# Kernel tuning notes

Measured on AMD Instinct MI355X. Metric: run time of the kernel, lower is better.

The kernel has to match this reference:

```python
import jax, jax.numpy as jnp
import numpy as np

B, S, H = 4, 4096, 2880
E, K = 32, 4


def setup_inputs() -> dict:
    key = jax.random.key(0)
    k1, k2 = jax.random.split(key)
    hidden_states = jax.random.normal(k1, (B, S, H), dtype=jnp.float32)
    # router weight, scaled like a typical init (std ~ 1/sqrt(H))
    weight = jax.random.normal(k2, (E, H), dtype=jnp.float32) / np.sqrt(H)
    bias = jnp.zeros((E,), dtype=jnp.float32)
    return {"hidden_states": hidden_states, "weight": weight, "bias": bias}


def reference(hidden_states, weight, bias):
    b, s, h = hidden_states.shape
    x = hidden_states.reshape(-1, h)                     # [T, H]
    logits = jnp.einsum('th,eh->te', x, weight) + bias   # [T, E]
    # select top-k logits (sorted descending), then softmax over the subset
    topk_logits, topk_idx = jax.lax.top_k(logits, K)     # [T, K]
    topk_weight = jax.nn.softmax(topk_logits.astype(jnp.float32), axis=-1)
    return topk_idx, topk_weight
```

## Files before the change

### kernel.cpp

```cpp
#include <hip/hip_runtime.h>
#include <math.h>

#define H_DIM 2880
#define E_NUM 32
#define TOPK 4
#define TT 256
#define HCHUNK 360
#define NCH 8
#define KS 20
#define NS (HCHUNK / KS)

#define GLD16(gp, lp)                                                  \
    __builtin_amdgcn_global_load_lds(                                  \
        (const __attribute__((address_space(1))) void*)(gp),           \
        (__attribute__((address_space(3))) void*)(lp), 16, 0, 0)

__global__ void transpose_w(const float* __restrict__ w, float* __restrict__ wt) {
    __shared__ float tile[32][33];
    const int h0 = blockIdx.x * 32;
    const int tx = threadIdx.x;
    const int ty = threadIdx.y;
    tile[tx][ty] = w[ty * H_DIM + h0 + tx];
    __syncthreads();
    wt[(h0 + ty) * E_NUM + tx] = tile[ty][tx];
}

__global__ __launch_bounds__(256, 2) void partial_logits(
    const float* __restrict__ x, const float* __restrict__ wt,
    float* __restrict__ part, int T) {
    __shared__ float xs[2][TT * KS];
    const int tid = threadIdx.x;
    const int t0 = blockIdx.x * TT;
    const int k0 = blockIdx.y * HCHUNK;
    const int wave = tid >> 6, lane = tid & 63;

    const float* g[5];
    int ldsoff[5];
#pragma unroll
    for (int i = 0; i < 5; ++i) {
        int f = wave * 320 + i * 64 + lane;
        int r = f / 5, c = f % 5;
        g[i] = x + (size_t)(t0 + r) * H_DIM + k0 + c * 4;
        ldsoff[i] = f * 4;
    }

    float acc[E_NUM];
#pragma unroll
    for (int e = 0; e < E_NUM; ++e) acc[e] = 0.0f;

    const float4* wt4 = (const float4*)wt;

#pragma unroll
    for (int i = 0; i < 5; ++i) GLD16(g[i], &xs[0][ldsoff[i]]);

    for (int s = 0; s < NS; ++s) {
        __syncthreads();
        if (s + 1 < NS) {
#pragma unroll
            for (int i = 0; i < 5; ++i)
                GLD16(g[i] + (size_t)(s + 1) * KS, &xs[(s + 1) & 1][ldsoff[i]]);
        }

        const float* xrow = &xs[s & 1][tid * KS];
        const int kbase = k0 + s * KS;
#pragma unroll
        for (int kk = 0; kk < KS / 4; ++kk) {
            float4 xv = *(const float4*)&xrow[kk * 4];
#pragma unroll
            for (int c = 0; c < 4; ++c) {
                float xk = (&xv.x)[c];
                int kg = kbase + kk * 4 + c;
#pragma unroll
                for (int j = 0; j < 8; ++j) {
                    float4 w4 = wt4[kg * 8 + j];
                    acc[j * 4 + 0] += xk * w4.x;
                    acc[j * 4 + 1] += xk * w4.y;
                    acc[j * 4 + 2] += xk * w4.z;
                    acc[j * 4 + 3] += xk * w4.w;
                }
            }
        }
    }

    float4* out4 = (float4*)(part + ((size_t)blockIdx.y * T + t0 + tid) * E_NUM);
#pragma unroll
    for (int j = 0; j < 8; ++j)
        out4[j] = make_float4(acc[j * 4 + 0], acc[j * 4 + 1], acc[j * 4 + 2], acc[j * 4 + 3]);
}

__global__ void topk_softmax(const float* __restrict__ part,
                             const float* __restrict__ bias,
                             float* __restrict__ out, int T) {
    const int t = blockIdx.x * 64 + threadIdx.x;
    if (t >= T) return;

    float logit[E_NUM];
    const float4* b4 = (const float4*)bias;
#pragma unroll
    for (int j = 0; j < 8; ++j) {
        float4 b = b4[j];
        logit[j * 4 + 0] = b.x; logit[j * 4 + 1] = b.y;
        logit[j * 4 + 2] = b.z; logit[j * 4 + 3] = b.w;
    }
    for (int hc = 0; hc < NCH; ++hc) {
        const float4* p4 = (const float4*)(part + ((size_t)hc * T + t) * E_NUM);
#pragma unroll
        for (int j = 0; j < 8; ++j) {
            float4 p = p4[j];
            logit[j * 4 + 0] += p.x; logit[j * 4 + 1] += p.y;
            logit[j * 4 + 2] += p.z; logit[j * 4 + 3] += p.w;
        }
    }

    int idx[TOPK];
    float val[TOPK];
#pragma unroll
    for (int k = 0; k < TOPK; ++k) {
        float best = -INFINITY;
        int bi = 0;
#pragma unroll
        for (int e = 0; e < E_NUM; ++e) {
            bool taken = false;
            for (int p = 0; p < k; ++p) taken = taken || (idx[p] == e);
            float v = logit[e];
            if (!taken && v > best) { best = v; bi = e; }
        }
        idx[k] = bi;
        val[k] = best;
    }

    float ex[TOPK], sum = 0.0f;
#pragma unroll
    for (int k = 0; k < TOPK; ++k) { ex[k] = expf(val[k] - val[0]); sum += ex[k]; }
    float inv = 1.0f / sum;

#pragma unroll
    for (int k = 0; k < TOPK; ++k) {
        out[(size_t)t * 4 + k] = (float)idx[k];
        out[(size_t)T * 4 + (size_t)t * 4 + k] = ex[k] * inv;
    }
}

extern "C" void kernel_launch(void* const* d_in, const int* in_sizes, int n_in,
                              void* d_out, int out_size, void* d_ws, size_t ws_size,
                              hipStream_t stream) {
    const float* x    = (const float*)d_in[0];
    const float* w    = (const float*)d_in[1];
    const float* bias = (const float*)d_in[2];
    float* out = (float*)d_out;

    const int T = in_sizes[0] / H_DIM;

    float* part = (float*)d_ws;
    float* wt = part + (size_t)NCH * T * E_NUM;

    transpose_w<<<dim3(H_DIM / 32), dim3(32, 32), 0, stream>>>(w, wt);
    partial_logits<<<dim3(T / TT, NCH), 256, 0, stream>>>(x, wt, part, T);
    topk_softmax<<<dim3((T + 63) / 64), 64, 0, stream>>>(part, bias, out, T);
}
```

Measured before the change: 318.8 us.

## Compute two tokens per thread with wide weight loads and parallelize partial reduction

```diff
diff --git a/kernel.cpp b/kernel.cpp
--- a/kernel.cpp
+++ b/kernel.cpp
@@ -4,11 +4,13 @@
 #define H_DIM 2880
 #define E_NUM 32
 #define TOPK 4
-#define TT 256
-#define HCHUNK 360
-#define NCH 8
-#define KS 20
-#define NS (HCHUNK / KS)
+#define NCH 16
+#define HCHUNK 180
+#define TB 512
+#define KS 12
+#define NS 15
+
+typedef float vf16 __attribute__((ext_vector_type(16)));
 
 #define GLD16(gp, lp)                                                  \
     __builtin_amdgcn_global_load_lds(                                  \
@@ -28,116 +30,138 @@
 __global__ __launch_bounds__(256, 2) void partial_logits(
     const float* __restrict__ x, const float* __restrict__ wt,
     float* __restrict__ part, int T) {
-    __shared__ float xs[2][TT * KS];
+    __shared__ float xs[2][TB * KS];
     const int tid = threadIdx.x;
-    const int t0 = blockIdx.x * TT;
+    const int t0 = blockIdx.x * TB;
     const int k0 = blockIdx.y * HCHUNK;
     const int wave = tid >> 6, lane = tid & 63;
 
-    const float* g[5];
-    int ldsoff[5];
+    const float* g[6];
+    int lo[6];
 #pragma unroll
-    for (int i = 0; i < 5; ++i) {
-        int f = wave * 320 + i * 64 + lane;
-        int r = f / 5, c = f % 5;
+    for (int i = 0; i < 6; ++i) {
+        int f = wave * 384 + i * 64 + lane;
+        int r = f / 3, c = f % 3;
         g[i] = x + (size_t)(t0 + r) * H_DIM + k0 + c * 4;
-        ldsoff[i] = f * 4;
+        lo[i] = f * 4;
     }
 
-    float acc[E_NUM];
+    float acc[64];
 #pragma unroll
-    for (int e = 0; e < E_NUM; ++e) acc[e] = 0.0f;
+    for (int e = 0; e < 64; ++e) acc[e] = 0.f;
 
-    const float4* wt4 = (const float4*)wt;
+    const vf16* wtv = (const vf16*)wt;
 
 #pragma unroll
-    for (int i = 0; i < 5; ++i) GLD16(g[i], &xs[0][ldsoff[i]]);
+    for (int i = 0; i < 6; ++i) GLD16(g[i], &xs[0][lo[i]]);
 
     for (int s = 0; s < NS; ++s) {
         __syncthreads();
         if (s + 1 < NS) {
 #pragma unroll
-            for (int i = 0; i < 5; ++i)
-                GLD16(g[i] + (size_t)(s + 1) * KS, &xs[(s + 1) & 1][ldsoff[i]]);
+            for (int i = 0; i < 6; ++i)
+                GLD16(g[i] + (size_t)(s + 1) * KS, &xs[(s + 1) & 1][lo[i]]);
         }
-
-        const float* xrow = &xs[s & 1][tid * KS];
-        const int kbase = k0 + s * KS;
+        const float* xa = &xs[s & 1][tid * KS];
+        const float* xb = &xs[s & 1][(tid + 256) * KS];
+        const int kb = k0 + s * KS;
 #pragma unroll
-        for (int kk = 0; kk < KS / 4; ++kk) {
-            float4 xv = *(const float4*)&xrow[kk * 4];
+        for (int kk = 0; kk < 3; ++kk) {
+            float4 va = *(const float4*)&xa[kk * 4];
+            float4 vb = *(const float4*)&xb[kk * 4];
 #pragma unroll
             for (int c = 0; c < 4; ++c) {
-                float xk = (&xv.x)[c];
-                int kg = kbase + kk * 4 + c;
+                float fa = (&va.x)[c], fb = (&vb.x)[c];
+                int kg = kb + kk * 4 + c;
+                vf16 w0 = wtv[kg * 2 + 0];
+                vf16 w1 = wtv[kg * 2 + 1];
 #pragma unroll
-                for (int j = 0; j < 8; ++j) {
-                    float4 w4 = wt4[kg * 8 + j];
-                    acc[j * 4 + 0] += xk * w4.x;
-                    acc[j * 4 + 1] += xk * w4.y;
-                    acc[j * 4 + 2] += xk * w4.z;
-                    acc[j * 4 + 3] += xk * w4.w;
+                for (int e = 0; e < 16; ++e) {
+                    acc[e]      += fa * w0[e];
+                    acc[16 + e] += fa * w1[e];
+                    acc[32 + e] += fb * w0[e];
+                    acc[48 + e] += fb * w1[e];
                 }
             }
         }
     }
 
-    float4* out4 = (float4*)(part + ((size_t)blockIdx.y * T + t0 + tid) * E_NUM);
+    float4* oa = (float4*)(part + ((size_t)blockIdx.y * T + t0 + tid) * E_NUM);
+    float4* ob = (float4*)(part + ((size_t)blockIdx.y * T + t0 + tid + 256) * E_NUM);
 #pragma unroll
-    for (int j = 0; j < 8; ++j)
-        out4[j] = make_float4(acc[j * 4 + 0], acc[j * 4 + 1], acc[j * 4 + 2], acc[j * 4 + 3]);
+    for (int j = 0; j < 8; ++j) {
+        oa[j] = make_float4(acc[j * 4], acc[j * 4 + 1], acc[j * 4 + 2], acc[j * 4 + 3]);
+        ob[j] = make_float4(acc[32 + j * 4], acc[32 + j * 4 + 1],
+                            acc[32 + j * 4 + 2], acc[32 + j * 4 + 3]);
+    }
 }
 
-__global__ void topk_softmax(const float* __restrict__ part,
-                             const float* __restrict__ bias,
-                             float* __restrict__ out, int T) {
-    const int t = blockIdx.x * 64 + threadIdx.x;
-    if (t >= T) return;
+__global__ __launch_bounds__(256) void topk_softmax(
+    const float* __restrict__ part, const float* __restrict__ bias,
+    float* __restrict__ out, int T) {
+    __shared__ float red[3][64][36];
+    const int tid = threadIdx.x, g = tid >> 6, l = tid & 63;
+    const int t = blockIdx.x * 64 + l;
 
-    float logit[E_NUM];
-    const float4* b4 = (const float4*)bias;
+    float s[E_NUM];
 #pragma unroll
-    for (int j = 0; j < 8; ++j) {
-        float4 b = b4[j];
-        logit[j * 4 + 0] = b.x; logit[j * 4 + 1] = b.y;
-        logit[j * 4 + 2] = b.z; logit[j * 4 + 3] = b.w;
-    }
-    for (int hc = 0; hc < NCH; ++hc) {
+    for (int e = 0; e < E_NUM; ++e) s[e] = 0.f;
+#pragma unroll
+    for (int q = 0; q < 4; ++q) {
+        const int hc = g * 4 + q;
         const float4* p4 = (const float4*)(part + ((size_t)hc * T + t) * E_NUM);
 #pragma unroll
         for (int j = 0; j < 8; ++j) {
             float4 p = p4[j];
-            logit[j * 4 + 0] += p.x; logit[j * 4 + 1] += p.y;
-            logit[j * 4 + 2] += p.z; logit[j * 4 + 3] += p.w;
+            s[j * 4] += p.x; s[j * 4 + 1] += p.y;
+            s[j * 4 + 2] += p.z; s[j * 4 + 3] += p.w;
         }
     }
+    if (g > 0) {
+#pragma unroll
+        for (int j = 0; j < 8; ++j)
+            *(float4*)&red[g - 1][l][j * 4] =
+                make_float4(s[j * 4], s[j * 4 + 1], s[j * 4 + 2], s[j * 4 + 3]);
+    }
+    __syncthreads();
+    if (g == 0) {
+        float logit[E_NUM];
+        const float4* b4 = (const float4*)bias;
+#pragma unroll
+        for (int j = 0; j < 8; ++j) {
+            float4 b = b4[j];
+            logit[j * 4] = b.x; logit[j * 4 + 1] = b.y;
+            logit[j * 4 + 2] = b.z; logit[j * 4 + 3] = b.w;
+        }
+#pragma unroll
+        for (int e = 0; e < E_NUM; ++e)
+            logit[e] += s[e] + red[0][l][e] + red[1][l][e] + red[2][l][e];
 
-    int idx[TOPK];
-    float val[TOPK];
+        int idx[TOPK];
+        float val[TOPK];
 #pragma unroll
-    for (int k = 0; k < TOPK; ++k) {
-        float best = -INFINITY;
-        int bi = 0;
+        for (int k = 0; k < TOPK; ++k) {
+            float best = -INFINITY;
+            int bi = 0;
 #pragma unroll
-        for (int e = 0; e < E_NUM; ++e) {
-            bool taken = false;
-            for (int p = 0; p < k; ++p) taken = taken || (idx[p] == e);
-            float v = logit[e];
-            if (!taken && v > best) { best = v; bi = e; }
+            for (int e = 0; e < E_NUM; ++e) {
+                bool taken = false;
+                for (int p = 0; p < k; ++p) taken = taken || (idx[p] == e);
+                float v = logit[e];
+                if (!taken && v > best) { best = v; bi = e; }
+            }
+            idx[k] = bi;
+            val[k] = best;
         }
-        idx[k] = bi;
-        val[k] = best;
-    }
-
-    float ex[TOPK], sum = 0.0f;
+        float ex[TOPK], sum = 0.f;
 #pragma unroll
-    for (int k = 0; k < TOPK; ++k) { ex[k] = expf(val[k] - val[0]); sum += ex[k]; }
-    float inv = 1.0f / sum;
-
+        for (int k = 0; k < TOPK; ++k) { ex[k] = expf(val[k] - val[0]); sum += ex[k]; }
+        float inv = 1.f / sum;
 #pragma unroll
-    for (int k = 0; k < TOPK; ++k) {
-        out[(size_t)t * 4 + k] = (float)idx[k];
-        out[(size_t)T * 4 + (size_t)t * 4 + k] = ex[k] * inv;
+        for (int k = 0; k < TOPK; ++k) {
+            out[(size_t)t * 4 + k] = (float)idx[k];
+            out[(size_t)T * 4 + (size_t)t * 4 + k] = ex[k] * inv;
+        }
     }
 }
 
@@ -155,6 +179,6 @@
     float* wt = part + (size_t)NCH * T * E_NUM;
 
     transpose_w<<<dim3(H_DIM / 32), dim3(32, 32), 0, stream>>>(w, wt);
-    partial_logits<<<dim3(T / TT, NCH), 256, 0, stream>>>(x, wt, part, T);
-    topk_softmax<<<dim3((T + 63) / 64), 64, 0, stream>>>(part, bias, out, T);
+    partial_logits<<<dim3(T / TB, NCH), 256, 0, stream>>>(x, wt, part, T);
+    topk_softmax<<<dim3(T / 64), 256, 0, stream>>>(part, bias, out, T);
 }
```

New measurement: 307.2 us. 1.04x faster.

## Fuse router GEMV and top-k softmax into one kernel with intra-block K split

Applied to the files above, without the earlier changes.

```diff
diff --git a/kernel.cpp b/kernel.cpp
--- a/kernel.cpp
+++ b/kernel.cpp
@@ -4,11 +4,13 @@
 #define H_DIM 2880
 #define E_NUM 32
 #define TOPK 4
-#define TT 256
-#define HCHUNK 360
-#define NCH 8
-#define KS 20
-#define NS (HCHUNK / KS)
+#define TT 64
+#define SW 144
+#define NSTG 20
+#define LROW 148
+#define SBUF (TT * LROW)
+
+typedef float vf16 __attribute__((ext_vector_type(16)));
 
 #define GLD16(gp, lp)                                                  \
     __builtin_amdgcn_global_load_lds(                                  \
@@ -25,119 +27,107 @@
     wt[(h0 + ty) * E_NUM + tx] = tile[ty][tx];
 }
 
-__global__ __launch_bounds__(256, 2) void partial_logits(
+__global__ __launch_bounds__(256) void gate_fused(
     const float* __restrict__ x, const float* __restrict__ wt,
-    float* __restrict__ part, int T) {
-    __shared__ float xs[2][TT * KS];
+    const float* __restrict__ bias, float* __restrict__ out, int T) {
+    __shared__ float smem[2 * SBUF];
     const int tid = threadIdx.x;
+    const int lane = tid & 63;
+    const int wq = __builtin_amdgcn_readfirstlane(tid >> 6);
     const int t0 = blockIdx.x * TT;
-    const int k0 = blockIdx.y * HCHUNK;
-    const int wave = tid >> 6, lane = tid & 63;
 
-    const float* g[5];
-    int ldsoff[5];
-#pragma unroll
-    for (int i = 0; i < 5; ++i) {
-        int f = wave * 320 + i * 64 + lane;
-        int r = f / 5, c = f % 5;
-        g[i] = x + (size_t)(t0 + r) * H_DIM + k0 + c * 4;
-        ldsoff[i] = f * 4;
-    }
+    const float* gbase = x + (size_t)(t0 + wq * 16) * H_DIM + lane * 4;
+    const bool act = (lane < 36);
 
     float acc[E_NUM];
 #pragma unroll
-    for (int e = 0; e < E_NUM; ++e) acc[e] = 0.0f;
-
-    const float4* wt4 = (const float4*)wt;
+    for (int e = 0; e < E_NUM; ++e) acc[e] = 0.f;
 
 #pragma unroll
-    for (int i = 0; i < 5; ++i) GLD16(g[i], &xs[0][ldsoff[i]]);
+    for (int i = 0; i < 16; ++i)
+        if (act) GLD16(gbase + (size_t)i * H_DIM, &smem[(wq * 16 + i) * LROW + lane * 4]);
 
-    for (int s = 0; s < NS; ++s) {
+    for (int s = 0; s < NSTG; ++s) {
         __syncthreads();
-        if (s + 1 < NS) {
+        if (s + 1 < NSTG) {
+            const float* gs = gbase + (size_t)(s + 1) * SW;
+            float* lb = &smem[((s + 1) & 1) * SBUF];
 #pragma unroll
-            for (int i = 0; i < 5; ++i)
-                GLD16(g[i] + (size_t)(s + 1) * KS, &xs[(s + 1) & 1][ldsoff[i]]);
+            for (int i = 0; i < 16; ++i)
+                if (act) GLD16(gs + (size_t)i * H_DIM, &lb[(wq * 16 + i) * LROW + lane * 4]);
         }
 
-        const float* xrow = &xs[s & 1][tid * KS];
-        const int kbase = k0 + s * KS;
+        const float* xrow = &smem[(s & 1) * SBUF + lane * LROW + wq * 36];
+        const int kb = s * SW + wq * 36;
 #pragma unroll
-        for (int kk = 0; kk < KS / 4; ++kk) {
-            float4 xv = *(const float4*)&xrow[kk * 4];
+        for (int j = 0; j < 9; ++j) {
+            float4 xv = *(const float4*)&xrow[j * 4];
 #pragma unroll
             for (int c = 0; c < 4; ++c) {
                 float xk = (&xv.x)[c];
-                int kg = kbase + kk * 4 + c;
+                const int kg = kb + j * 4 + c;
+                vf16 w0 = *(const vf16*)(wt + (size_t)kg * E_NUM);
+                vf16 w1 = *(const vf16*)(wt + (size_t)kg * E_NUM + 16);
 #pragma unroll
-                for (int j = 0; j < 8; ++j) {
-                    float4 w4 = wt4[kg * 8 + j];
-                    acc[j * 4 + 0] += xk * w4.x;
-                    acc[j * 4 + 1] += xk * w4.y;
-                    acc[j * 4 + 2] += xk * w4.z;
-                    acc[j * 4 + 3] += xk * w4.w;
+                for (int e = 0; e < 16; ++e) {
+                    acc[e]      += xk * w0[e];
+                    acc[16 + e] += xk * w1[e];
                 }
             }
         }
     }
 
-    float4* out4 = (float4*)(part + ((size_t)blockIdx.y * T + t0 + tid) * E_NUM);
+    float* red = smem;
 #pragma unroll
     for (int j = 0; j < 8; ++j)
-        out4[j] = make_float4(acc[j * 4 + 0], acc[j * 4 + 1], acc[j * 4 + 2], acc[j * 4 + 3]);
-}
+        *(float4*)&red[wq * 2304 + lane * 36 + j * 4] =
+            make_float4(acc[j * 4], acc[j * 4 + 1], acc[j * 4 + 2], acc[j * 4 + 3]);
+    __syncthreads();
 
-__global__ void topk_softmax(const float* __restrict__ part,
-                             const float* __restrict__ bias,
-                             float* __restrict__ out, int T) {
-    const int t = blockIdx.x * 64 + threadIdx.x;
-    if (t >= T) return;
-
-    float logit[E_NUM];
-    const float4* b4 = (const float4*)bias;
-#pragma unroll
-    for (int j = 0; j < 8; ++j) {
-        float4 b = b4[j];
-        logit[j * 4 + 0] = b.x; logit[j * 4 + 1] = b.y;
-        logit[j * 4 + 2] = b.z; logit[j * 4 + 3] = b.w;
-    }
-    for (int hc = 0; hc < NCH; ++hc) {
-        const float4* p4 = (const float4*)(part + ((size_t)hc * T + t) * E_NUM);
+    if (wq == 0) {
+        const int t = t0 + lane;
+        float logit[E_NUM];
+        const float4* b4 = (const float4*)bias;
 #pragma unroll
         for (int j = 0; j < 8; ++j) {
-            float4 p = p4[j];
-            logit[j * 4 + 0] += p.x; logit[j * 4 + 1] += p.y;
-            logit[j * 4 + 2] += p.z; logit[j * 4 + 3] += p.w;
+            float4 b = b4[j];
+            logit[j * 4] = b.x; logit[j * 4 + 1] = b.y;
+            logit[j * 4 + 2] = b.z; logit[j * 4 + 3] = b.w;
         }
-    }
+#pragma unroll
+        for (int g = 0; g < 4; ++g)
+#pragma unroll
+            for (int j = 0; j < 8; ++j) {
+                float4 v = *(const float4*)&red[g * 2304 + lane * 36 + j * 4];
+                logit[j * 4] += v.x; logit[j * 4 + 1] += v.y;
+                logit[j * 4 + 2] += v.z; logit[j * 4 + 3] += v.w;
+            }
 
-    int idx[TOPK];
-    float val[TOPK];
+        int idx[TOPK];
+        float val[TOPK];
 #pragma unroll
-    for (int k = 0; k < TOPK; ++k) {
-        float best = -INFINITY;
-        int bi = 0;
+        for (int k = 0; k < TOPK; ++k) {
+            float best = -INFINITY;
+            int bi = 0;
 #pragma unroll
-        for (int e = 0; e < E_NUM; ++e) {
-            bool taken = false;
-            for (int p = 0; p < k; ++p) taken = taken || (idx[p] == e);
-            float v = logit[e];
-            if (!taken && v > best) { best = v; bi = e; }
+            for (int e = 0; e < E_NUM; ++e) {
+                bool taken = false;
+                for (int p = 0; p < k; ++p) taken = taken || (idx[p] == e);
+                float v = logit[e];
+                if (!taken && v > best) { best = v; bi = e; }
+            }
+            idx[k] = bi;
+            val[k] = best;
         }
-        idx[k] = bi;
-        val[k] = best;
-    }
-
-    float ex[TOPK], sum = 0.0f;
+        float ex[TOPK], sum = 0.f;
 #pragma unroll
-    for (int k = 0; k < TOPK; ++k) { ex[k] = expf(val[k] - val[0]); sum += ex[k]; }
-    float inv = 1.0f / sum;
-
+        for (int k = 0; k < TOPK; ++k) { ex[k] = expf(val[k] - val[0]); sum += ex[k]; }
+        float inv = 1.f / sum;
 #pragma unroll
-    for (int k = 0; k < TOPK; ++k) {
-        out[(size_t)t * 4 + k] = (float)idx[k];
-        out[(size_t)T * 4 + (size_t)t * 4 + k] = ex[k] * inv;
+        for (int k = 0; k < TOPK; ++k) {
+            out[(size_t)t * 4 + k] = (float)idx[k];
+            out[(size_t)T * 4 + (size_t)t * 4 + k] = ex[k] * inv;
+        }
     }
 }
 
@@ -151,10 +141,8 @@
 
     const int T = in_sizes[0] / H_DIM;
 
-    float* part = (float*)d_ws;
-    float* wt = part + (size_t)NCH * T * E_NUM;
+    float* wt = (float*)d_ws;
 
     transpose_w<<<dim3(H_DIM / 32), dim3(32, 32), 0, stream>>>(w, wt);
-    partial_logits<<<dim3(T / TT, NCH), 256, 0, stream>>>(x, wt, part, T);
-    topk_softmax<<<dim3((T + 63) / 64), 64, 0, stream>>>(part, bias, out, T);
+    gate_fused<<<dim3(T / TT), 256, 0, stream>>>(x, wt, bias, out, T);
 }
```

New measurement: 386.0 us. 1.21x slower.
